# Kernel tuning notes

Hardware: AMD Instinct MI355X
Metric: run time of the kernel (lower is better)

The kernel has to match this reference:

```python
import jax, jax.numpy as jnp
import numpy as np

N_NODES = 50000
N_EDGES = 1600000
N_FEAT = 128
EMB = 128
N_CLASSES = 10
N_GRAPHS = 512


def setup_inputs() -> dict:
    key = jax.random.key(0)
    ks = jax.random.split(key, 12)
    x = jax.random.normal(ks[0], (N_NODES, N_FEAT), dtype=jnp.float32)
    edge_index = jax.random.randint(ks[1], (2, N_EDGES), 0, N_NODES, dtype=jnp.int64)
    batch = jnp.sort(jax.random.randint(ks[2], (N_NODES,), 0, N_GRAPHS, dtype=jnp.int64))
    def glorot(k, fan_in, fan_out):
        lim = jnp.sqrt(6.0 / (fan_in + fan_out)).astype(jnp.float32)
        return jax.random.uniform(k, (fan_in, fan_out), jnp.float32, -lim, lim)
    W0 = glorot(ks[3], N_FEAT, EMB); b0 = jnp.zeros((EMB,), jnp.float32)
    W1 = glorot(ks[4], EMB, EMB);    b1 = jnp.zeros((EMB,), jnp.float32)
    W2 = glorot(ks[5], EMB, EMB);    b2 = jnp.zeros((EMB,), jnp.float32)
    Wout = glorot(ks[6], EMB, N_CLASSES)
    bout = jnp.zeros((N_CLASSES,), jnp.float32)
    return {"x": x, "edge_index": edge_index, "batch": batch,
            "W0": W0, "b0": b0, "W1": W1, "b1": b1, "W2": W2, "b2": b2,
            "Wout": Wout, "bout": bout}


def _gcn_conv(x, W, b, src, dst, norm, n_nodes):
    # PyG GCNConv: h = x @ W; aggregate norm * h[src] into dst; add bias.
    h = x @ W                                  # [N, out]
    msg = h[src] * norm[:, None]               # [E+N, out] gather (incl. self-loops)
    out = jax.ops.segment_sum(msg, dst, num_segments=n_nodes)
    return out + b


def reference(x, edge_index, batch, W0, b0, W1, b1, W2, b2, Wout, bout):
    n_nodes = x.shape[0]
    # add self-loops (GCNConv default add_self_loops=True)
    loops = jnp.arange(n_nodes, dtype=edge_index.dtype)
    src = jnp.concatenate([edge_index[0], loops])
    dst = jnp.concatenate([edge_index[1], loops])
    # symmetric normalization D^{-1/2} (A+I) D^{-1/2}
    deg = jax.ops.segment_sum(jnp.ones_like(dst, dtype=x.dtype), dst,
                              num_segments=n_nodes)
    deg_inv_sqrt = jnp.where(deg > 0, jax.lax.rsqrt(jnp.maximum(deg, 1.0)), 0.0)
    norm = deg_inv_sqrt[src] * deg_inv_sqrt[dst]   # [E+N]
    out = jnp.tanh(_gcn_conv(x, W0, b0, src, dst, norm, n_nodes))
    out = jnp.tanh(_gcn_conv(out, W1, b1, src, dst, norm, n_nodes))
    out = _gcn_conv(out, W2, b2, src, dst, norm, n_nodes)
    # global mean pool over per-node graph ids
    sums = jax.ops.segment_sum(out, batch, num_segments=N_GRAPHS)
    counts = jax.ops.segment_sum(jnp.ones((n_nodes,), out.dtype), batch,
                                 num_segments=N_GRAPHS)
    pooled = sums / jnp.maximum(counts, 1.0)[:, None]   # [G, EMB]
    logits = pooled @ Wout + bout                        # [G, C]
    return jax.nn.log_softmax(logits, axis=1)
```

## Files before the change

kernel.cpp:

```cpp
#include <hip/hip_runtime.h>
#include <math.h>


#define BLK_EDGES 4096
#define MAXB 128
#define ECAP 4096
#define NPB 8
#define WS_STRIDE 136

typedef __attribute__((ext_vector_type(8))) short bf16x8;
typedef __attribute__((ext_vector_type(4))) float f32x4;
typedef __attribute__((ext_vector_type(2))) float f32x2;

static __device__ inline unsigned short f2bf(float f) {
    unsigned u = __float_as_uint(f);
    unsigned r = (u + 0x7FFFu + ((u >> 16) & 1u)) >> 16;
    return (unsigned short)r;
}
static __device__ inline float bf_lo(unsigned u) { return __uint_as_float(u << 16); }
static __device__ inline float bf_hi(unsigned u) { return __uint_as_float(u & 0xFFFF0000u); }
static __device__ inline unsigned char f2fp8(float v) {
    v = fminf(fmaxf(v, -240.f), 240.f);
    int u = __builtin_amdgcn_cvt_pk_fp8_f32(v, v, 0, false);
    return (unsigned char)(u & 0xFF);
}
static __device__ inline float fast_tanh(float x) {
    float ax = fabsf(x);
    float e = __expf(2.0f * ax);
    float r = fmaf(-2.0f, __builtin_amdgcn_rcpf(e + 1.0f), 1.0f);
    return copysignf(r, x);
}

__global__ __launch_bounds__(256) void blk_hist_prep(const int* __restrict__ dst,
        int* __restrict__ histT, int E, int NBLK, int NB,
        const float* __restrict__ W0, const float* __restrict__ W1,
        const float* __restrict__ W2, unsigned short* __restrict__ wt0,
        unsigned short* __restrict__ wt1, unsigned short* __restrict__ wt2,
        unsigned char* __restrict__ hs, int N) {
    __shared__ int h[MAXB];
    int blk = blockIdx.x, t = threadIdx.x;
    if (blk >= NBLK) {
        if (blk == NBLK && t < 32)
            ((unsigned*)(hs + (size_t)N * 128))[t] = 0u;
        int i = (blk - NBLK) * 256 + t;
        int w = i >> 14, j = i & 16383;
        int k = j >> 7, n2 = j & 127;
        const float* Wp = (w == 0) ? W0 : (w == 1) ? W1 : W2;
        unsigned short* Wt = (w == 0) ? wt0 : (w == 1) ? wt1 : wt2;
        Wt[n2 * 128 + k] = f2bf(Wp[k * 128 + n2]);
        return;
    }
    for (int i = t; i < NB; i += 256) h[i] = 0;
    __syncthreads();
    int lo = blk * BLK_EDGES;
    int hi = min(E, lo + BLK_EDGES);
    for (int i = lo + t; i < hi; i += 256)
        atomicAdd(&h[dst[i] >> 9], 1);
    __syncthreads();
    for (int i = t; i < NB; i += 256) histT[i * NBLK + blk] = h[i];
}

__global__ void scan_block(const int* __restrict__ cnt, int* __restrict__ off,
                           int* __restrict__ bsum, int n) {
    __shared__ int lds[256];
    int t = threadIdx.x;
    int i = blockIdx.x * 256 + t;
    int v = (i < n) ? cnt[i] : 0;
    lds[t] = v;
    __syncthreads();
    for (int d = 1; d < 256; d <<= 1) {
        int add = (t >= d) ? lds[t - d] : 0;
        __syncthreads();
        lds[t] += add;
        __syncthreads();
    }
    if (i < n) off[i] = lds[t] - v;
    if (t == 255) bsum[blockIdx.x] = lds[255];
}

__global__ void scan_top(const int* __restrict__ bsum, int* __restrict__ boff,
                         int nblocks) {
    __shared__ int lds[256];
    int t = threadIdx.x;
    int v = (t < nblocks) ? bsum[t] : 0;
    lds[t] = v;
    __syncthreads();
    for (int d = 1; d < 256; d <<= 1) {
        int add = (t >= d) ? lds[t - d] : 0;
        __syncthreads();
        lds[t] += add;
        __syncthreads();
    }
    if (t < nblocks) boff[t] = lds[t] - v;
}

__global__ __launch_bounds__(256) void scatter_packed(const int* __restrict__ src,
        const int* __restrict__ dst, const int* __restrict__ P,
        const int* __restrict__ boff, unsigned* __restrict__ packed,
        int E, int NBLK, int NB) {
    __shared__ int cur[MAXB];
    int blk = blockIdx.x, t = threadIdx.x;
    for (int i = t; i < NB; i += 256) {
        int idx = i * NBLK + blk;
        cur[i] = P[idx] + boff[idx >> 8];
    }
    __syncthreads();
    int lo = blk * BLK_EDGES;
    int hi = min(E, lo + BLK_EDGES);
    for (int i = lo + t; i < hi; i += 256) {
        int d = dst[i];
        int pos = atomicAdd(&cur[d >> 9], 1);
        packed[pos] = ((unsigned)d << 16) | (unsigned)src[i];
    }
}

__global__ __launch_bounds__(256) void bucket_build(const unsigned* __restrict__ packed,
        const int* __restrict__ P, const int* __restrict__ boff, int* __restrict__ off,
        float* __restrict__ dis, unsigned short* __restrict__ csr16,
        int E, int NBLK, int N, int NB) {
    __shared__ int cnt[512];
    __shared__ int loc[512];
    __shared__ int ps[256];
    int b = blockIdx.x, t = threadIdx.x;
    int i0 = b * NBLK, i1 = (b + 1) * NBLK;
    int start = P[i0] + boff[i0 >> 8];
    int end   = (b == NB - 1) ? E : (P[i1] + boff[i1 >> 8]);
    cnt[t] = 0; cnt[t + 256] = 0;
    __syncthreads();
    for (int i = start + t; i < end; i += 256)
        atomicAdd(&cnt[(packed[i] >> 16) & 511], 1);
    __syncthreads();
    int c0 = cnt[2 * t], c1 = cnt[2 * t + 1];
    ps[t] = c0 + c1;
    __syncthreads();
    for (int d = 1; d < 256; d <<= 1) {
        int add = (t >= d) ? ps[t - d] : 0;
        __syncthreads();
        ps[t] += add;
        __syncthreads();
    }
    int pexcl = ps[t] - (c0 + c1);
    loc[2 * t]     = start + pexcl;
    loc[2 * t + 1] = start + pexcl + c0;
    __syncthreads();
    int node0 = b * 512;
    for (int l = t; l < 512; l += 256) {
        int node = node0 + l;
        if (node < N) {
            off[node] = loc[l];
            dis[node] = rsqrtf((float)cnt[l] + 1.0f);
        }
    }
    if (b == NB - 1 && t == 0) off[N] = E;
    __syncthreads();
    for (int i = start + t; i < end; i += 256) {
        unsigned p = packed[i];
        int l = (p >> 16) & 511;
        int pos = atomicAdd(&loc[l], 1);
        csr16[pos] = (unsigned short)(p & 0xFFFFu);
    }
}

template<int IN_F32>
__global__ __launch_bounds__(256) void gemm_mfma(const void* __restrict__ Av,
        const unsigned short* __restrict__ Wt, const float* __restrict__ dis,
        unsigned char* __restrict__ Hs8, int n) {
    __shared__ unsigned short Ws[128 * WS_STRIDE];
    int t = threadIdx.x;
    for (int i = t; i < 128 * 16; i += 256) {
        int r = i >> 4, j = i & 15;
        uint4 u = ((const uint4*)(Wt + r * 128))[j];
        *(uint4*)&Ws[r * WS_STRIDE + j * 8] = u;
    }
    __syncthreads();

    int wave = t >> 6, lane = t & 63;
    int quad = lane >> 4, l16 = lane & 15;
    int row0 = blockIdx.x * 128 + wave * 32;

    int ra0 = row0 + l16;      if (ra0 >= n) ra0 = n - 1;
    int ra1 = row0 + 16 + l16; if (ra1 >= n) ra1 = n - 1;

    f32x4 acc[2][8];
    const f32x4 z = {0.f, 0.f, 0.f, 0.f};
#pragma unroll
    for (int mi = 0; mi < 2; ++mi)
#pragma unroll
        for (int ni = 0; ni < 8; ++ni) acc[mi][ni] = z;

#pragma unroll
    for (int ks = 0; ks < 4; ++ks) {
        int kof = ks * 32 + quad * 8;
        bf16x8 a0, a1;
        if (IN_F32) {
            const float* A0 = (const float*)Av + (size_t)ra0 * 128 + kof;
            const float* A1 = (const float*)Av + (size_t)ra1 * 128 + kof;
            float4 p0 = ((const float4*)A0)[0], p1 = ((const float4*)A0)[1];
            float4 q0 = ((const float4*)A1)[0], q1 = ((const float4*)A1)[1];
            a0[0] = (short)f2bf(p0.x); a0[1] = (short)f2bf(p0.y);
            a0[2] = (short)f2bf(p0.z); a0[3] = (short)f2bf(p0.w);
            a0[4] = (short)f2bf(p1.x); a0[5] = (short)f2bf(p1.y);
            a0[6] = (short)f2bf(p1.z); a0[7] = (short)f2bf(p1.w);
            a1[0] = (short)f2bf(q0.x); a1[1] = (short)f2bf(q0.y);
            a1[2] = (short)f2bf(q0.z); a1[3] = (short)f2bf(q0.w);
            a1[4] = (short)f2bf(q1.x); a1[5] = (short)f2bf(q1.y);
            a1[6] = (short)f2bf(q1.z); a1[7] = (short)f2bf(q1.w);
        } else {
            a0 = *(const bf16x8*)((const unsigned short*)Av + (size_t)ra0 * 128 + kof);
            a1 = *(const bf16x8*)((const unsigned short*)Av + (size_t)ra1 * 128 + kof);
        }
        bf16x8 b[8];
#pragma unroll
        for (int ni = 0; ni < 8; ++ni)
            b[ni] = *(const bf16x8*)&Ws[(ni * 16 + l16) * WS_STRIDE + kof];
#pragma unroll
        for (int ni = 0; ni < 8; ++ni) {
            acc[0][ni] = __builtin_amdgcn_mfma_f32_16x16x32_bf16(a0, b[ni], acc[0][ni], 0, 0, 0);
            acc[1][ni] = __builtin_amdgcn_mfma_f32_16x16x32_bf16(a1, b[ni], acc[1][ni], 0, 0, 0);
        }
    }
#pragma unroll
    for (int mi = 0; mi < 2; ++mi) {
        int rb = row0 + mi * 16 + quad * 4;
#pragma unroll
        for (int reg = 0; reg < 4; ++reg) {
            int r = rb + reg;
            if (r < n) {
                float dv = dis[r];
#pragma unroll
                for (int ni = 0; ni < 8; ++ni)
                    Hs8[(size_t)r * 128 + ni * 16 + l16] = f2fp8(acc[mi][ni][reg] * dv);
            }
        }
    }
}

template<int DO_TANH>
__global__ __launch_bounds__(512) void aggregate3(const unsigned char* __restrict__ hs,
    const unsigned short* __restrict__ csr, const int* __restrict__ off,
    const float* __restrict__ dis, const float* __restrict__ bias,
    unsigned* __restrict__ outp, int n) {
    __shared__ unsigned short eidx[ECAP + 16];
    int t = threadIdx.x;
    int node0 = blockIdx.x * NPB;
    int b0 = off[node0];
    int top = node0 + NPB < n ? node0 + NPB : n;
    int bN = off[top];
    int mblk = bN - b0;
    bool staged = (mblk <= ECAP);
    if (staged)
        for (int i = t; i < mblk; i += 512) eidx[i] = csr[b0 + i];
    __syncthreads();

    int node = node0 + (t >> 6);
    if (node >= n) return;
    int lane = t & 63;
    int g = lane >> 4;
    int fq = lane & 15;
    unsigned fob = (unsigned)fq << 3;

    int e0 = off[node];
    int e1 = off[node + 1];
    int le0 = e0 - b0;
    int m = e1 - e0;

    unsigned sv = *(const unsigned short*)(hs + (((unsigned)node) << 7) + fob + 2 * g);

    float a0 = 0.f, a1 = 0.f, a2 = 0.f, a3 = 0.f;
    float a4 = 0.f, a5 = 0.f, a6 = 0.f, a7 = 0.f;
    auto cadd = [&](uint2 v) {
        f32x2 p0 = __builtin_amdgcn_cvt_pk_f32_fp8((int)v.x, false);
        f32x2 p1 = __builtin_amdgcn_cvt_pk_f32_fp8((int)v.x, true);
        f32x2 p2 = __builtin_amdgcn_cvt_pk_f32_fp8((int)v.y, false);
        f32x2 p3 = __builtin_amdgcn_cvt_pk_f32_fp8((int)v.y, true);
        a0 += p0.x; a1 += p0.y; a2 += p1.x; a3 += p1.y;
        a4 += p2.x; a5 += p2.y; a6 += p3.x; a7 += p3.y;
    };
    uint2 va[4], vb[4];
    auto sumB = [&](uint2* v) {
#pragma unroll
        for (int j = 0; j < 4; ++j) cadd(v[j]);
    };
    auto loadL = [&](int i, uint2* v) {
#pragma unroll
        for (int j = 0; j < 4; ++j) {
            int e = i + g + 4 * j;
            int idx = eidx[le0 + e];
            idx = (e < m) ? idx : n;
            v[j] = *(const uint2*)(hs + ((unsigned)idx << 7) + fob);
        }
    };
    auto loadG = [&](int i, uint2* v) {
#pragma unroll
        for (int j = 0; j < 4; ++j) {
            int e = i + g + 4 * j;
            int idx = csr[e0 + e];
            idx = (e < m) ? idx : n;
            v[j] = *(const uint2*)(hs + ((unsigned)idx << 7) + fob);
        }
    };

    int B = (m + 15) >> 4;
    if (B) {
        if (staged) {
            loadL(0, va);
            int k = 1;
            for (; k + 1 < B; k += 2) {
                loadL(k << 4, vb);       sumB(va);
                loadL((k + 1) << 4, va); sumB(vb);
            }
            if (k < B) { loadL(k << 4, vb); sumB(va); sumB(vb); }
            else       { sumB(va); }
        } else {
            loadG(0, va);
            int k = 1;
            for (; k + 1 < B; k += 2) {
                loadG(k << 4, vb);       sumB(va);
                loadG((k + 1) << 4, va); sumB(vb);
            }
            if (k < B) { loadG(k << 4, vb); sumB(va); sumB(vb); }
            else       { sumB(va); }
        }
    }

    a0 += __shfl_xor(a0, 32, 64); a0 += __shfl_xor(a0, 16, 64);
    a1 += __shfl_xor(a1, 32, 64); a1 += __shfl_xor(a1, 16, 64);
    a2 += __shfl_xor(a2, 32, 64); a2 += __shfl_xor(a2, 16, 64);
    a3 += __shfl_xor(a3, 32, 64); a3 += __shfl_xor(a3, 16, 64);
    a4 += __shfl_xor(a4, 32, 64); a4 += __shfl_xor(a4, 16, 64);
    a5 += __shfl_xor(a5, 32, 64); a5 += __shfl_xor(a5, 16, 64);
    a6 += __shfl_xor(a6, 32, 64); a6 += __shfl_xor(a6, 16, 64);
    a7 += __shfl_xor(a7, 32, 64); a7 += __shfl_xor(a7, 16, 64);

    float s0 = (g & 2) ? ((g & 1) ? a6 : a4) : ((g & 1) ? a2 : a0);
    float s1 = (g & 2) ? ((g & 1) ? a7 : a5) : ((g & 1) ? a3 : a1);
    f32x2 sf = __builtin_amdgcn_cvt_pk_f32_fp8((int)sv, false);
    s0 += sf.x;
    s1 += sf.y;
    float dn = dis[node];
    float2 bv = ((const float2*)bias)[fq * 4 + g];
    float o0 = fmaf(dn, s0, bv.x);
    float o1 = fmaf(dn, s1, bv.y);
    if (DO_TANH) { o0 = fast_tanh(o0); o1 = fast_tanh(o1); }
    unsigned o = (unsigned)f2bf(o0) | ((unsigned)f2bf(o1) << 16);
    outp[(size_t)node * 64 + fq * 4 + g] = o;
}

__global__ __launch_bounds__(256) void pool_head(const unsigned* __restrict__ actb,
    const int* __restrict__ batch, const float* __restrict__ Wout,
    const float* __restrict__ bout, float* __restrict__ out, int n, int C) {
    __shared__ float psum[4][128];
    __shared__ float l[16];
    __shared__ float stats[2];
    int g = blockIdx.x;
    int t = threadIdx.x;
    int w = t >> 6;
    int lane = t & 63;
    int lo = 0, hi = n;
    while (lo < hi) { int mid = (lo + hi) >> 1; if (batch[mid] < g) lo = mid + 1; else hi = mid; }
    int lo1 = lo, hi1 = n;
    while (lo1 < hi1) { int mid = (lo1 + hi1) >> 1; if (batch[mid] < g + 1) lo1 = mid + 1; else hi1 = mid; }
    float ax = 0.f, ay = 0.f;
    for (int i = lo + w; i < lo1; i += 4) {
        unsigned v = actb[(size_t)i * 64 + lane];
        ax += bf_lo(v);
        ay += bf_hi(v);
    }
    psum[w][2 * lane]     = ax;
    psum[w][2 * lane + 1] = ay;
    __syncthreads();
    if (w == 0) {
        int cnt = lo1 - lo;
        float inv = 1.0f / (float)(cnt > 0 ? cnt : 1);
        float sx = (psum[0][2 * lane] + psum[1][2 * lane])
                 + (psum[2][2 * lane] + psum[3][2 * lane]);
        float sy = (psum[0][2 * lane + 1] + psum[1][2 * lane + 1])
                 + (psum[2][2 * lane + 1] + psum[3][2 * lane + 1]);
        psum[0][2 * lane]     = sx * inv;
        psum[0][2 * lane + 1] = sy * inv;
    }
    __syncthreads();
    if (t < C) {
        float acc = bout[t];
        for (int f = 0; f < 128; ++f)
            acc = fmaf(psum[0][f], Wout[(size_t)f * C + t], acc);
        l[t] = acc;
    }
    __syncthreads();
    if (t == 0) {
        float m = -1e30f;
        for (int c = 0; c < C; ++c) m = fmaxf(m, l[c]);
        float s = 0.f;
        for (int c = 0; c < C; ++c) s += expf(l[c] - m);
        stats[0] = m;
        stats[1] = logf(s);
    }
    __syncthreads();
    if (t < C) out[(size_t)g * C + t] = l[t] - stats[0] - stats[1];
}

extern "C" void kernel_launch(void* const* d_in, const int* in_sizes, int n_in,
                              void* d_out, int out_size, void* d_ws, size_t ws_size,
                              hipStream_t stream) {
    const float* x     = (const float*)d_in[0];
    const int*   edge  = (const int*)d_in[1];
    const int*   batch = (const int*)d_in[2];
    const float* W0 = (const float*)d_in[3];
    const float* b0 = (const float*)d_in[4];
    const float* W1 = (const float*)d_in[5];
    const float* b1 = (const float*)d_in[6];
    const float* W2 = (const float*)d_in[7];
    const float* b2 = (const float*)d_in[8];
    const float* Wout = (const float*)d_in[9];
    const float* bout = (const float*)d_in[10];
    float* out = (float*)d_out;

    const int N = in_sizes[0] / 128;
    const int E = in_sizes[1] / 2;
    const int C = in_sizes[10];
    const int G = out_size / C;

    const int* src = edge;
    const int* dst = edge + E;

    const int NBLK = (E + BLK_EDGES - 1) / BLK_EDGES;
    const int NB   = (N + 511) / 512;
    const int NBQ  = NB * NBLK;
    const int PREPB = (3 * 16384) / 256;

    char* p = (char*)d_ws;
    auto alloc = [&](size_t bytes) -> void* {
        void* r = (void*)p;
        p += (bytes + 255) & ~(size_t)255;
        return r;
    };
    unsigned char* hs = (unsigned char*)alloc((size_t)(N + 1) * 128);
    unsigned* actb = (unsigned*)alloc((size_t)N * 128 * 2);
    float* dis    = (float*)alloc((size_t)N * 4);
    int*   off    = (int*)alloc((size_t)(N + 1) * 4);
    int*   P      = (int*)alloc((size_t)(NBQ + 1) * 4);
    int*   bsum   = (int*)alloc(256 * 4);
    int*   boff   = (int*)alloc(256 * 4);
    unsigned* packed = (unsigned*)alloc((size_t)E * 4);
    unsigned short* csr16 = (unsigned short*)alloc((size_t)(E + 16) * 2);
    unsigned short* wt0 = (unsigned short*)alloc(128 * 128 * 2);
    unsigned short* wt1 = (unsigned short*)alloc(128 * 128 * 2);
    unsigned short* wt2 = (unsigned short*)alloc(128 * 128 * 2);

    const int sb = (NBQ + 255) / 256;

    blk_hist_prep<<<NBLK + PREPB, 256, 0, stream>>>(dst, P, E, NBLK, NB,
                                                    W0, W1, W2, wt0, wt1, wt2,
                                                    hs, N);
    scan_block<<<sb, 256, 0, stream>>>(P, P, bsum, NBQ);
    scan_top<<<1, 256, 0, stream>>>(bsum, boff, sb);
    scatter_packed<<<NBLK, 256, 0, stream>>>(src, dst, P, boff, packed, E, NBLK, NB);
    bucket_build<<<NB, 256, 0, stream>>>(packed, P, boff, off, dis, csr16, E, NBLK, N, NB);

    const int gb = (N + 127) / 128;
    const int ab = (N + NPB - 1) / NPB;

    gemm_mfma<1><<<gb, 256, 0, stream>>>(x,    wt0, dis, hs, N);
    aggregate3<1><<<ab, 512, 0, stream>>>(hs, csr16, off, dis, b0, actb, N);
    gemm_mfma<0><<<gb, 256, 0, stream>>>(actb, wt1, dis, hs, N);
    aggregate3<1><<<ab, 512, 0, stream>>>(hs, csr16, off, dis, b1, actb, N);
    gemm_mfma<0><<<gb, 256, 0, stream>>>(actb, wt2, dis, hs, N);
    aggregate3<0><<<ab, 512, 0, stream>>>(hs, csr16, off, dis, b2, actb, N);

    pool_head<<<G, 256, 0, stream>>>(actb, batch, Wout, bout, out, N, C);
}
```

Baseline: 306.8 us.

## Shrink GEMM row tile to 64 and drop LDS edge staging in aggregation

The GEMM now assigns 16 rows per wave (64 rows per block) instead of 32, halving accumulator registers and doubling the grid so more blocks run at once. The aggregation kernel no longer stages each block's CSR indices into shared memory and reads them straight from global memory, which removes the __syncthreads barrier and the shared allocation. The trade is that each GEMM block reloads the weight tile for half as many rows, and aggregation index reads go to global memory and cache instead of LDS.

```diff
diff --git a/kernel.cpp b/kernel.cpp
--- a/kernel.cpp
+++ b/kernel.cpp
@@ -4,7 +4,6 @@
 
 #define BLK_EDGES 4096
 #define MAXB 128
-#define ECAP 4096
 #define NPB 8
 #define WS_STRIDE 136
 
@@ -176,61 +175,46 @@
 
     int wave = t >> 6, lane = t & 63;
     int quad = lane >> 4, l16 = lane & 15;
-    int row0 = blockIdx.x * 128 + wave * 32;
-
-    int ra0 = row0 + l16;      if (ra0 >= n) ra0 = n - 1;
-    int ra1 = row0 + 16 + l16; if (ra1 >= n) ra1 = n - 1;
-
-    f32x4 acc[2][8];
+    int row0 = blockIdx.x * 64 + wave * 16;
+
+    int ra0 = row0 + l16; if (ra0 >= n) ra0 = n - 1;
+
+    f32x4 acc[8];
     const f32x4 z = {0.f, 0.f, 0.f, 0.f};
 #pragma unroll
-    for (int mi = 0; mi < 2; ++mi)
-#pragma unroll
-        for (int ni = 0; ni < 8; ++ni) acc[mi][ni] = z;
+    for (int ni = 0; ni < 8; ++ni) acc[ni] = z;
 
 #pragma unroll
     for (int ks = 0; ks < 4; ++ks) {
         int kof = ks * 32 + quad * 8;
-        bf16x8 a0, a1;
+        bf16x8 a0;
         if (IN_F32) {
             const float* A0 = (const float*)Av + (size_t)ra0 * 128 + kof;
-            const float* A1 = (const float*)Av + (size_t)ra1 * 128 + kof;
             float4 p0 = ((const float4*)A0)[0], p1 = ((const float4*)A0)[1];
-            float4 q0 = ((const float4*)A1)[0], q1 = ((const float4*)A1)[1];
             a0[0] = (short)f2bf(p0.x); a0[1] = (short)f2bf(p0.y);
             a0[2] = (short)f2bf(p0.z); a0[3] = (short)f2bf(p0.w);
             a0[4] = (short)f2bf(p1.x); a0[5] = (short)f2bf(p1.y);
             a0[6] = (short)f2bf(p1.z); a0[7] = (short)f2bf(p1.w);
-            a1[0] = (short)f2bf(q0.x); a1[1] = (short)f2bf(q0.y);
-            a1[2] = (short)f2bf(q0.z); a1[3] = (short)f2bf(q0.w);
-            a1[4] = (short)f2bf(q1.x); a1[5] = (short)f2bf(q1.y);
-            a1[6] = (short)f2bf(q1.z); a1[7] = (short)f2bf(q1.w);
         } else {
             a0 = *(const bf16x8*)((const unsigned short*)Av + (size_t)ra0 * 128 + kof);
-            a1 = *(const bf16x8*)((const unsigned short*)Av + (size_t)ra1 * 128 + kof);
         }
         bf16x8 b[8];
 #pragma unroll
         for (int ni = 0; ni < 8; ++ni)
             b[ni] = *(const bf16x8*)&Ws[(ni * 16 + l16) * WS_STRIDE + kof];
 #pragma unroll
-        for (int ni = 0; ni < 8; ++ni) {
-            acc[0][ni] = __builtin_amdgcn_mfma_f32_16x16x32_bf16(a0, b[ni], acc[0][ni], 0, 0, 0);
-            acc[1][ni] = __builtin_amdgcn_mfma_f32_16x16x32_bf16(a1, b[ni], acc[1][ni], 0, 0, 0);
-        }
-    }
-#pragma unroll
-    for (int mi = 0; mi < 2; ++mi) {
-        int rb = row0 + mi * 16 + quad * 4;
-#pragma unroll
-        for (int reg = 0; reg < 4; ++reg) {
-            int r = rb + reg;
-            if (r < n) {
-                float dv = dis[r];
-#pragma unroll
-                for (int ni = 0; ni < 8; ++ni)
-                    Hs8[(size_t)r * 128 + ni * 16 + l16] = f2fp8(acc[mi][ni][reg] * dv);
-            }
+        for (int ni = 0; ni < 8; ++ni)
+            acc[ni] = __builtin_amdgcn_mfma_f32_16x16x32_bf16(a0, b[ni], acc[ni], 0, 0, 0);
+    }
+    int rb = row0 + quad * 4;
+#pragma unroll
+    for (int reg = 0; reg < 4; ++reg) {
+        int r = rb + reg;
+        if (r < n) {
+            float dv = dis[r];
+#pragma unroll
+            for (int ni = 0; ni < 8; ++ni)
+                Hs8[(size_t)r * 128 + ni * 16 + l16] = f2fp8(acc[ni][reg] * dv);
         }
     }
 }
@@ -240,19 +224,8 @@
     const unsigned short* __restrict__ csr, const int* __restrict__ off,
     const float* __restrict__ dis, const float* __restrict__ bias,
     unsigned* __restrict__ outp, int n) {
-    __shared__ unsigned short eidx[ECAP + 16];
     int t = threadIdx.x;
-    int node0 = blockIdx.x * NPB;
-    int b0 = off[node0];
-    int top = node0 + NPB < n ? node0 + NPB : n;
-    int bN = off[top];
-    int mblk = bN - b0;
-    bool staged = (mblk <= ECAP);
-    if (staged)
-        for (int i = t; i < mblk; i += 512) eidx[i] = csr[b0 + i];
-    __syncthreads();
-
-    int node = node0 + (t >> 6);
+    int node = blockIdx.x * NPB + (t >> 6);
     if (node >= n) return;
     int lane = t & 63;
     int g = lane >> 4;
@@ -261,7 +234,6 @@
 
     int e0 = off[node];
     int e1 = off[node + 1];
-    int le0 = e0 - b0;
     int m = e1 - e0;
 
     unsigned sv = *(const unsigned short*)(hs + (((unsigned)node) << 7) + fob + 2 * g);
@@ -281,16 +253,7 @@
 #pragma unroll
         for (int j = 0; j < 4; ++j) cadd(v[j]);
     };
-    auto loadL = [&](int i, uint2* v) {
-#pragma unroll
-        for (int j = 0; j < 4; ++j) {
-            int e = i + g + 4 * j;
-            int idx = eidx[le0 + e];
-            idx = (e < m) ? idx : n;
-            v[j] = *(const uint2*)(hs + ((unsigned)idx << 7) + fob);
-        }
-    };
-    auto loadG = [&](int i, uint2* v) {
+    auto loadB = [&](int i, uint2* v) {
 #pragma unroll
         for (int j = 0; j < 4; ++j) {
             int e = i + g + 4 * j;
@@ -302,25 +265,14 @@
 
     int B = (m + 15) >> 4;
     if (B) {
-        if (staged) {
-            loadL(0, va);
-            int k = 1;
-            for (; k + 1 < B; k += 2) {
-                loadL(k << 4, vb);       sumB(va);
-                loadL((k + 1) << 4, va); sumB(vb);
-            }
-            if (k < B) { loadL(k << 4, vb); sumB(va); sumB(vb); }
-            else       { sumB(va); }
-        } else {
-            loadG(0, va);
-            int k = 1;
-            for (; k + 1 < B; k += 2) {
-                loadG(k << 4, vb);       sumB(va);
-                loadG((k + 1) << 4, va); sumB(vb);
-            }
-            if (k < B) { loadG(k << 4, vb); sumB(va); sumB(vb); }
-            else       { sumB(va); }
+        loadB(0, va);
+        int k = 1;
+        for (; k + 1 < B; k += 2) {
+            loadB(k << 4, vb);       sumB(va);
+            loadB((k + 1) << 4, va); sumB(vb);
         }
+        if (k < B) { loadB(k << 4, vb); sumB(va); sumB(vb); }
+        else       { sumB(va); }
     }
 
     a0 += __shfl_xor(a0, 32, 64); a0 += __shfl_xor(a0, 16, 64);
@@ -457,7 +409,7 @@
     scatter_packed<<<NBLK, 256, 0, stream>>>(src, dst, P, boff, packed, E, NBLK, NB);
     bucket_build<<<NB, 256, 0, stream>>>(packed, P, boff, off, dis, csr16, E, NBLK, N, NB);
 
-    const int gb = (N + 127) / 128;
+    const int gb = (N + 63) / 64;
     const int ab = (N + NPB - 1) / NPB;
 
     gemm_mfma<1><<<gb, 256, 0, stream>>>(x,    wt0, dis, hs, N);
```

After: 357.7 us. 1.17x slower.
